# Performance work log

Hardware: AMD Instinct MI355X
Metric: run time of the kernel (lower is better)

The kernel has to match this reference:

```python
import jax, jax.numpy as jnp
import numpy as np

SP = 1024; H = 128; W = 128; BAND = 224; DIM = 256; HEADS = 8; DH = 64; HID = 512; NS = 6
SCALE = DH ** -0.5

def setup_inputs() -> dict:
    key = jax.random.key(0)
    ks = iter(jax.random.split(key, 48))
    def rn(shape, s=0.02):
        return jax.random.normal(next(ks), shape, dtype=jnp.float32) * s
    # pixel -> superpixel one-hot assignment; every column nonempty so C_T division is safe
    Q = jax.nn.one_hot(jnp.arange(H * W) % SP, SP, dtype=jnp.float32)
    A = rn((SP, SP), 0.1)  # additive attention bias (graph prior)
    T1 = jax.random.normal(next(ks), (1, BAND, H, W), dtype=jnp.float32)
    T2 = jax.random.normal(next(ks), (1, BAND, H, W), dtype=jnp.float32)
    return {
        "T1": T1, "T2": T2, "Q": Q, "A": A,
        "convW_in": rn((2, 256, BAND, 3, 3)), "convB_in": jnp.zeros((2, 256), jnp.float32),
        "convW": rn((5, 2, 256, 256, 3, 3)), "convB": jnp.zeros((5, 2, 256), jnp.float32),
        "fc0_W": rn((2, BAND + 256, 256)), "fc0_b": jnp.zeros((2, 256), jnp.float32),
        "fc_W": rn((5, 2, 512, 256)), "fc_b": jnp.zeros((5, 2, 256), jnp.float32),
        "pos": rn((NS, 2, SP, DIM)),
        "ln1_g": jnp.ones((NS, 2, DIM), jnp.float32), "ln1_b": jnp.zeros((NS, 2, DIM), jnp.float32),
        "qkv_W": rn((NS, 2, DIM, 3 * HEADS * DH)),
        "out_W": rn((NS, 2, HEADS * DH, DIM)), "out_b": jnp.zeros((NS, 2, DIM), jnp.float32),
        "ln2_g": jnp.ones((NS, 2, DIM), jnp.float32), "ln2_b": jnp.zeros((NS, 2, DIM), jnp.float32),
        "ff_W1": rn((NS, 2, DIM, HID)), "ff_b1": jnp.zeros((NS, 2, HID), jnp.float32),
        "ff_W2": rn((NS, 2, HID, DIM)), "ff_b2": jnp.zeros((NS, 2, DIM), jnp.float32),
        "head_W1": rn((DIM, 128)), "head_b1": jnp.zeros((128,), jnp.float32),
        "head_W2": rn((128, 2)), "head_b2": jnp.zeros((2,), jnp.float32),
    }

def _ln(x, g, b):
    m = jnp.mean(x, -1, keepdims=True)
    v = jnp.mean((x - m) ** 2, -1, keepdims=True)
    return (x - m) * jax.lax.rsqrt(v + 1e-5) * g + b

def _conv(x, w, b):
    y = jax.lax.conv_general_dilated(x, w, (1, 1), 'SAME', dimension_numbers=('NCHW', 'OIHW', 'NCHW'))
    return y + b[None, :, None, None]

def _ct(Q, img):
    # superpixel mean pooling: (Q^T @ pixels) / |superpixel|
    band = img.shape[1]
    x = jnp.transpose(img, (0, 2, 3, 1)).reshape(-1, band)  # (HW, band)
    out = (Q.T @ x) / jnp.sum(Q, axis=0)[:, None]
    return out[None]  # (1, SP, band)

def _encoder(x, A, pos, g1, b1, qkvW, oW, ob, g2, b2, w1, bb1, w2, bb2):
    x = x + pos[None]
    h = _ln(x, g1, b1)
    q, k, v = jnp.split(h @ qkvW, 3, axis=-1)
    split = lambda t: t.reshape(1, SP, HEADS, DH).transpose(0, 2, 1, 3)
    q, k, v = split(q), split(k), split(v)
    dots = jnp.einsum('bhid,bhjd->bhij', q, k) * SCALE + A  # bias added pre-softmax
    attn = jax.nn.softmax(dots, axis=-1)
    o = jnp.einsum('bhij,bhjd->bhid', attn, v).transpose(0, 2, 1, 3).reshape(1, SP, HEADS * DH)
    x = x + o @ oW + ob
    h2 = _ln(x, g2, b2)
    return x + jax.nn.gelu(h2 @ w1 + bb1, approximate=False) @ w2 + bb2

def reference(T1, T2, Q, A, convW_in, convB_in, convW, convB, fc0_W, fc0_b, fc_W, fc_b, pos, ln1_g, ln1_b, qkv_W, out_W, out_b, ln2_g, ln2_b, ff_W1, ff_b1, ff_W2, ff_b2, head_W1, head_b1, head_W2, head_b2):
    def enc(t, s, br):
        return _encoder(t, A, pos[s, br], ln1_g[s, br], ln1_b[s, br], qkv_W[s, br], out_W[s, br], out_b[s, br], ln2_g[s, br], ln2_b[s, br], ff_W1[s, br], ff_b1[s, br], ff_W2[s, br], ff_b2[s, br])
    LS = [_ct(Q, T1), _ct(Q, T2)]
    c = [_conv(T1, convW_in[0], convB_in[0]), _conv(T2, convW_in[1], convB_in[1])]
    x = [None, None]
    for br in range(2):
        cat = jnp.concatenate([_ct(Q, c[br]), LS[br]], axis=-1)  # (1, SP, 256+224)
        x[br] = enc(jax.nn.relu(cat) @ fc0_W[br] + fc0_b[br], 0, br)
    for s in range(1, NS):
        for br in range(2):
            c[br] = _conv(c[br], convW[s - 1, br], convB[s - 1, br])
            cat = jnp.concatenate([_ct(Q, c[br]), x[br]], axis=-1)  # (1, SP, 512)
            x[br] = enc(jax.nn.relu(cat) @ fc_W[s - 1, br] + fc_b[s - 1, br], s, br)
    d = jnp.abs(x[0] - x[1])[0]  # (SP, DIM) change feature
    h = jax.nn.relu(d @ head_W1 + head_b1)
    return jax.nn.softmax(h @ head_W2 + head_b2, axis=1)  # (SP, 2)
```

## Files before the change

### kernel.cpp

```cpp
#include <hip/hip_runtime.h>
#include <hip/hip_bf16.h>
#include <math.h>

#define SPX 1024
#define HW 16384

typedef short short8 __attribute__((ext_vector_type(8)));
typedef short short4v __attribute__((ext_vector_type(4)));
typedef float f32x4 __attribute__((ext_vector_type(4)));

__device__ inline short f2bf(float v){ union{ __hip_bfloat16 h; short s; } u; u.h = __float2bfloat16(v); return u.s; }
__device__ inline float bf2f(short s){ union{ __hip_bfloat16 h; short t; } u; u.t = s; return __bfloat162float(u.h); }

#define GLL(gp, lp) __builtin_amdgcn_global_load_lds( \
    (const __attribute__((address_space(1))) void*)(gp), \
    (__attribute__((address_space(3))) void*)(lp), 16, 0, 0)

__global__ __launch_bounds__(256) void megaprep_k(
    const float* __restrict__ T1, const float* __restrict__ T2,
    const float* __restrict__ cwin, const float* __restrict__ cw,
    const float* __restrict__ qkvW, const float* __restrict__ outW,
    const float* __restrict__ ff1W, const float* __restrict__ ff2W,
    const float* __restrict__ fcW, const float* __restrict__ fc0W,
    short* __restrict__ wt0, short* __restrict__ wtl, short* __restrict__ zbuf,
    short* __restrict__ thwc, float* __restrict__ LSb,
    short* __restrict__ qkvWT, short* __restrict__ outWT,
    short* __restrict__ ff1T, short* __restrict__ ff2T,
    short* __restrict__ fcT, short* __restrict__ fc0WT)
{
    __shared__ float tile[32][33];
    int bid = blockIdx.x;
    int tid = threadIdx.x;
    if (bid < 27072) {
        long long idx = (long long)bid * 256 + tid;
        if (idx < 64) zbuf[idx] = 0;
        const long long n0 = 2LL * 256 * 2016;
        if (idx < n0) {
            int br = (int)(idx / (256 * 2016)); int rem = (int)(idx % (256 * 2016));
            int co = rem / 2016; int k = rem % 2016;
            int tap = k / 224, ci = k % 224;
            wt0[idx] = f2bf(cwin[((size_t)(br * 256 + co) * 224 + ci) * 9 + tap]);
        } else {
            long long i2 = idx - n0;
            if (i2 < 10LL * 256 * 2304) {
                int l = (int)(i2 / (256 * 2304)); int rem = (int)(i2 % (256 * 2304));
                int co = rem / 2304; int k = rem % 2304;
                int tap = k / 256, ci = k % 256;
                wtl[i2] = f2bf(cw[((size_t)(l * 256 + co) * 256 + ci) * 9 + tap]);
            }
        }
        return;
    }
    bid -= 27072;
    if (bid < 28672) {
        long long idx = (long long)bid * 256 + tid;
        int br = (int)(idx / 3670016LL); int rem = (int)(idx % 3670016LL);
        int p = rem / 224, c = rem % 224;
        const float* src = br ? T2 : T1;
        thwc[idx] = f2bf(src[(size_t)c * HW + p]);
        return;
    }
    bid -= 28672;
    if (bid < 1792) {
        int idx = bid * 256 + tid;
        int z = idx / 229376; int rem = idx % 229376;
        int c = rem >> 10, s = rem & 1023;
        const float* src = z ? T2 : T1;
        const float* p = src + (size_t)c * HW + s;
        float acc = 0.f;
#pragma unroll
        for (int j = 0; j < 16; ++j) acc += p[j * 1024];
        LSb[(size_t)z * 229376 + (size_t)s * 224 + c] = acc * (1.f / 16.f);
        return;
    }
    bid -= 1792;
    const float* src; short* dst; int K, N, nx;
    if (bid < 4608)                        { src = qkvW; dst = qkvWT; K = 256; N = 1536; nx = 48; }
    else { bid -= 4608; if (bid < 1536)    { src = outW; dst = outWT; K = 512; N = 256;  nx = 8; }
    else { bid -= 1536; if (bid < 1536)    { src = ff1W; dst = ff1T;  K = 256; N = 512;  nx = 16; }
    else { bid -= 1536; if (bid < 1536)    { src = ff2W; dst = ff2T;  K = 512; N = 256;  nx = 8; }
    else { bid -= 1536; if (bid < 1280)    { src = fcW;  dst = fcT;   K = 512; N = 256;  nx = 8; }
    else { bid -= 1280;                      src = fc0W; dst = fc0WT; K = 480; N = 256;  nx = 8; } } } } }
    int per = nx * (K >> 5);
    int b = bid / per, rem = bid % per;
    int n0 = (rem % nx) * 32, k0 = (rem / nx) * 32;
    const float* s = src + (size_t)b * K * N;
    short* d = dst + (size_t)b * K * N;
    int r = tid >> 3, c4 = (tid & 7) * 4;
    float4 v = *(const float4*)(s + (size_t)(k0 + r) * N + n0 + c4);
    tile[r][c4 + 0] = v.x; tile[r][c4 + 1] = v.y; tile[r][c4 + 2] = v.z; tile[r][c4 + 3] = v.w;
    __syncthreads();
    short4v o;
#pragma unroll
    for (int i = 0; i < 4; ++i) o[i] = f2bf(tile[c4 + i][r]);
    *(short4v*)(d + (size_t)(n0 + r) * K + k0 + c4) = o;
}

__global__ __launch_bounds__(256, 3) void conv_mfma_k(
    const short* __restrict__ inB, long long inStride,
    const short* __restrict__ wtB, long long wtStride,
    const float* __restrict__ biasB, long long biasStride,
    short* __restrict__ outB, long long outStride,
    const short* __restrict__ zbuf, int Cin)
{
    __shared__ short Ah[3 * 4160];
    int id = blockIdx.x;
    int x7 = id & 7, t = id >> 3;
    int br = x7 & 1;
    int y = (x7 >> 1) * 32 + (t >> 1);
    int co0 = (t & 1) * 128;
    const short* in = inB + (size_t)br * inStride;
    const short* wt = wtB + (size_t)br * wtStride;
    const float* bias = biasB + (size_t)br * biasStride;
    short* out = outB + (size_t)br * outStride;
    int tid = threadIdx.x;
    int lane = tid & 63, w = tid >> 6;
    int wm = w >> 1, wn = w & 1;
    int lrow = lane >> 2, lsub = (lane & 3) * 8;
    int mrow = lane & 15, quad = lane >> 4, kg = quad * 8;
    int Kw = 9 * Cin;
    if (tid < 96) {
        int dy = tid >> 5, ci = tid & 31;
        Ah[dy * 4160 + ci] = 0;
        Ah[dy * 4160 + 129 * 32 + ci] = 0;
    }
    f32x4 acc[4][4];
#pragma unroll
    for (int i = 0; i < 4; ++i)
#pragma unroll
        for (int j = 0; j < 4; ++j) acc[i][j] = (f32x4){0.f, 0.f, 0.f, 0.f};

    const short* wbase[4];
#pragma unroll
    for (int j = 0; j < 4; ++j)
        wbase[j] = wt + (size_t)(co0 + wn * 64 + j * 16 + mrow) * Kw + kg;

    auto stageA = [&](int cc) {
        int c8 = cc * 32;
#pragma unroll
        for (int g = 0; g < 6; ++g) {
            int idg = g * 4 + w;
            int dy = idg >> 3, grp = idg & 7;
            int gy = y + dy - 1;
            const short* gp = ((unsigned)gy < 128u)
                ? in + ((size_t)(gy * 128 + grp * 16 + lrow) * Cin + c8 + lsub)
                : zbuf + lsub;
            GLL(gp, Ah + dy * 4160 + (1 + grp * 16) * 32);
        }
    };

    short8 Bcur[4], Bnxt[4];
#pragma unroll
    for (int j = 0; j < 4; ++j) Bcur[j] = *(const short8*)(wbase[j]);
    stageA(0);
    __syncthreads();
    int NC = Cin >> 5;
    for (int cc = 0; cc < NC; ++cc) {
        int cbase = cc * 32;
#pragma unroll
        for (int tap = 0; tap < 9; ++tap) {
            if (tap < 8) {
#pragma unroll
                for (int j = 0; j < 4; ++j)
                    Bnxt[j] = *(const short8*)(wbase[j] + (tap + 1) * Cin + cbase);
            } else if (cc + 1 < NC) {
#pragma unroll
                for (int j = 0; j < 4; ++j)
                    Bnxt[j] = *(const short8*)(wbase[j] + cbase + 32);
            }
            const short* Ap = Ah + (tap / 3) * 4160 + (tap % 3) * 32;
            short8 af[4];
#pragma unroll
            for (int i = 0; i < 4; ++i)
                af[i] = *(const short8*)(Ap + (wm * 64 + i * 16 + mrow) * 32 + kg);
#pragma unroll
            for (int i = 0; i < 4; ++i)
#pragma unroll
                for (int j = 0; j < 4; ++j)
                    acc[i][j] = __builtin_amdgcn_mfma_f32_16x16x32_bf16(af[i], Bcur[j], acc[i][j], 0, 0, 0);
#pragma unroll
            for (int j = 0; j < 4; ++j) Bcur[j] = Bnxt[j];
        }
        if (cc + 1 < NC) {
            __syncthreads();
            stageA(cc + 1);
            __syncthreads();
        }
    }
    int ln15 = lane & 15;
    float bj[4];
#pragma unroll
    for (int j = 0; j < 4; ++j) bj[j] = bias[co0 + wn * 64 + j * 16 + ln15];
#pragma unroll
    for (int i = 0; i < 4; ++i) {
#pragma unroll
        for (int r = 0; r < 4; ++r) {
            int px = wm * 64 + i * 16 + quad * 4 + r;
            size_t po = ((size_t)y * 128 + px) * 256 + co0 + wn * 64 + ln15;
#pragma unroll
            for (int j = 0; j < 4; ++j)
                out[po + j * 16] = f2bf(acc[i][j][r] + bj[j]);
        }
    }
}

__global__ __launch_bounds__(256) void gemm64_k(
    const short* __restrict__ A, long long sA, int lda,
    const short* __restrict__ Bt, long long sB, int K,
    float* Cf, long long sCf, short* Cb, long long sCb, int ldc,
    const float* __restrict__ bias, long long sBias,
    const float* addm, long long sAdd, int ldadd, int act)
{
    __shared__ short Asm[2][2048];
    __shared__ short Bsm[2][2048];
    int z = blockIdx.z;
    const short* Ap = A + (size_t)z * sA;
    const short* Bp = Bt + (size_t)z * sB;
    const float* biasp = bias ? bias + (size_t)z * sBias : nullptr;
    const float* addp = addm ? addm + (size_t)z * sAdd : nullptr;
    int bn = blockIdx.x * 64, bm = blockIdx.y * 64;
    int tid = threadIdx.x;
    int lane = tid & 63, w = tid >> 6;
    int wm = w >> 1, wn = w & 1;
    int rr = tid >> 2, lsub = (tid & 3) * 8;
    f32x4 acc[2][2];
#pragma unroll
    for (int i = 0; i < 2; ++i)
#pragma unroll
        for (int j = 0; j < 2; ++j) acc[i][j] = (f32x4){0.f, 0.f, 0.f, 0.f};

    auto stage = [&](int k0, int p) {
        GLL(Ap + (size_t)(bm + rr) * lda + k0 + lsub, Asm[p] + (w * 16) * 32);
        GLL(Bp + (size_t)(bn + rr) * K + k0 + lsub, Bsm[p] + (w * 16) * 32);
    };
    stage(0, 0);
    __syncthreads();
    int p = 0;
    int mrow = lane & 15, kg = (lane >> 4) * 8;
    for (int k0 = 0; k0 < K; k0 += 32) {
        if (k0 + 32 < K) stage(k0 + 32, p ^ 1);
        short8 af[2], bfr[2];
#pragma unroll
        for (int i = 0; i < 2; ++i)
            af[i] = *(const short8*)(Asm[p] + (wm * 32 + i * 16 + mrow) * 32 + kg);
#pragma unroll
        for (int j = 0; j < 2; ++j)
            bfr[j] = *(const short8*)(Bsm[p] + (wn * 32 + j * 16 + mrow) * 32 + kg);
#pragma unroll
        for (int i = 0; i < 2; ++i)
#pragma unroll
            for (int j = 0; j < 2; ++j)
                acc[i][j] = __builtin_amdgcn_mfma_f32_16x16x32_bf16(af[i], bfr[j], acc[i][j], 0, 0, 0);
        __syncthreads();
        p ^= 1;
    }
    int ln15 = lane & 15, quad = lane >> 4;
    float* Cfp = Cf ? Cf + (size_t)z * sCf : nullptr;
    short* Cbp = Cb ? Cb + (size_t)z * sCb : nullptr;
#pragma unroll
    for (int i = 0; i < 2; ++i) {
#pragma unroll
        for (int r = 0; r < 4; ++r) {
            int row = bm + wm * 32 + i * 16 + quad * 4 + r;
            long long ro = (long long)row * ldc;
#pragma unroll
            for (int j = 0; j < 2; ++j) {
                int col = bn + wn * 32 + j * 16 + ln15;
                float v = acc[i][j][r];
                if (biasp) v += biasp[col];
                if (addp) v += addp[(long long)row * ldadd + col];
                if (act == 1) v = fmaxf(v, 0.f);
                else if (act == 2) v = 0.5f * v * (1.f + erff(v * 0.70710678118f));
                if (Cfp) Cfp[ro + col] = v;
                if (Cbp) Cbp[ro + col] = f2bf(v);
            }
        }
    }
}

__global__ __launch_bounds__(256) void gemm_ln_k(
    const short* __restrict__ A, long long sA, int lda,
    const short* __restrict__ Bt, long long sB, int K,
    const float* __restrict__ bias, long long sBias,
    const float* __restrict__ addm, long long sAdd,
    const float* __restrict__ g, const float* __restrict__ b,
    float* __restrict__ xout, long long sX, short* __restrict__ hout, long long sH)
{
    __shared__ short As[2][512];
    __shared__ short Bsm[2][8192];
    __shared__ float redS[16][4], redQ[16][4];
    int z = blockIdx.y;
    int bm = blockIdx.x * 16;
    const short* Ap = A + (size_t)z * sA;
    const short* Bp = Bt + (size_t)z * sB;
    const float* biasp = bias + (size_t)z * sBias;
    const float* addp = addm + (size_t)z * sAdd;
    const float* gp = g + (size_t)z * 256;
    const float* bp = b + (size_t)z * 256;
    float* xo = xout + (size_t)z * sX;
    short* ho = hout + (size_t)z * sH;
    int tid = threadIdx.x;
    int lane = tid & 63, w = tid >> 6;
    int lrow = lane >> 2, lsub = (lane & 3) * 8;
    int mrow = lane & 15, quad = lane >> 4, kg = quad * 8;
    f32x4 acc[4];
#pragma unroll
    for (int j = 0; j < 4; ++j) acc[j] = (f32x4){0.f, 0.f, 0.f, 0.f};

    auto stage = [&](int k0, int p) {
        if (w == 0) GLL(Ap + (size_t)(bm + lrow) * lda + k0 + lsub, As[p]);
#pragma unroll
        for (int s = 0; s < 4; ++s) {
            int r0 = (w * 4 + s) * 16;
            GLL(Bp + (size_t)(r0 + lrow) * K + k0 + lsub, Bsm[p] + r0 * 32);
        }
    };
    stage(0, 0);
    __syncthreads();
    int NK = K >> 5, p = 0;
    for (int kk = 0; kk < NK; ++kk) {
        if (kk + 1 < NK) stage((kk + 1) * 32, p ^ 1);
        short8 af = *(const short8*)(As[p] + mrow * 32 + kg);
#pragma unroll
        for (int j = 0; j < 4; ++j) {
            short8 bfr = *(const short8*)(Bsm[p] + (w * 64 + j * 16 + mrow) * 32 + kg);
            acc[j] = __builtin_amdgcn_mfma_f32_16x16x32_bf16(af, bfr, acc[j], 0, 0, 0);
        }
        __syncthreads();
        p ^= 1;
    }
    float v[4][4], s4[4], q4[4];
#pragma unroll
    for (int r = 0; r < 4; ++r) { s4[r] = 0.f; q4[r] = 0.f; }
#pragma unroll
    for (int j = 0; j < 4; ++j) {
        int col = w * 64 + j * 16 + mrow;
        float bb = biasp[col];
#pragma unroll
        for (int r = 0; r < 4; ++r) {
            int row = bm + quad * 4 + r;
            float val = acc[j][r] + bb + addp[(size_t)row * 256 + col];
            v[j][r] = val;
            s4[r] += val;
            q4[r] += val * val;
        }
    }
#pragma unroll
    for (int r = 0; r < 4; ++r) {
#pragma unroll
        for (int msk = 1; msk < 16; msk <<= 1) {
            s4[r] += __shfl_xor(s4[r], msk);
            q4[r] += __shfl_xor(q4[r], msk);
        }
    }
    if (mrow == 0) {
#pragma unroll
        for (int r = 0; r < 4; ++r) {
            redS[quad * 4 + r][w] = s4[r];
            redQ[quad * 4 + r][w] = q4[r];
        }
    }
    __syncthreads();
#pragma unroll
    for (int r = 0; r < 4; ++r) {
        int r16 = quad * 4 + r;
        float S = redS[r16][0] + redS[r16][1] + redS[r16][2] + redS[r16][3];
        float Q = redQ[r16][0] + redQ[r16][1] + redQ[r16][2] + redQ[r16][3];
        float m = S * (1.f / 256.f);
        float var = Q * (1.f / 256.f) - m * m;
        float rs = rsqrtf(var + 1e-5f);
        size_t ro = (size_t)(bm + r16) * 256;
#pragma unroll
        for (int j = 0; j < 4; ++j) {
            int col = w * 64 + j * 16 + mrow;
            xo[ro + col] = v[j][r];
            ho[ro + col] = f2bf((v[j][r] - m) * rs * gp[col] + bp[col]);
        }
    }
}

__global__ __launch_bounds__(256) void flash_k(const short* __restrict__ qkv, const float* __restrict__ Abias,
                                               short* __restrict__ obuf)
{
    __shared__ short Qs[64 * 72];
    __shared__ short Ks[128 * 72];
    __shared__ short Vt[64 * 136];
    __shared__ short Ps[64 * 136];
    int q0 = blockIdx.x * 64, h = blockIdx.y, br = blockIdx.z;
    const short* qb = qkv + (size_t)br * 1572864;
    int tid = threadIdx.x;
    int lane = tid & 63, w = tid >> 6;
    int ln15 = lane & 15, quad = lane >> 4;
    {
        int row = tid & 63, c0 = (tid >> 6) * 16;
        const short* src = qb + (size_t)(q0 + row) * 1536 + h * 64 + c0;
        *(short8*)(Qs + row * 72 + c0) = *(const short8*)src;
        *(short8*)(Qs + row * 72 + c0 + 8) = *(const short8*)(src + 8);
    }
    f32x4 Oc[4];
    float mrow[4], lsum[4];
#pragma unroll
    for (int i = 0; i < 4; ++i) { Oc[i] = (f32x4){0.f, 0.f, 0.f, 0.f}; mrow[i] = -1e30f; lsum[i] = 0.f; }

    for (int j = 0; j < 8; ++j) {
        int k0 = j * 128;
        {
            int row = tid & 127, half = tid >> 7;
            const short* ks = qb + (size_t)(k0 + row) * 1536 + 512 + h * 64 + half * 32;
#pragma unroll
            for (int g = 0; g < 4; ++g)
                *(short8*)(Ks + row * 72 + half * 32 + g * 8) = *(const short8*)(ks + g * 8);
            const short* vs = qb + (size_t)(k0 + row) * 1536 + 1024 + h * 64 + half * 32;
#pragma unroll
            for (int g = 0; g < 4; ++g) {
                short8 vv = *(const short8*)(vs + g * 8);
#pragma unroll
                for (int e = 0; e < 8; ++e)
                    Vt[(half * 32 + g * 8 + e) * 136 + row] = vv[e];
            }
        }
        __syncthreads();
        short8 aq[2];
#pragma unroll
        for (int g = 0; g < 2; ++g)
            aq[g] = *(const short8*)(Qs + (w * 16 + ln15) * 72 + g * 32 + quad * 8);
        f32x4 Sf[8];
#pragma unroll
        for (int nf = 0; nf < 8; ++nf) Sf[nf] = (f32x4){0.f, 0.f, 0.f, 0.f};
#pragma unroll
        for (int nf = 0; nf < 8; ++nf)
#pragma unroll
            for (int g = 0; g < 2; ++g) {
                short8 bk = *(const short8*)(Ks + (nf * 16 + ln15) * 72 + g * 32 + quad * 8);
                Sf[nf] = __builtin_amdgcn_mfma_f32_16x16x32_bf16(aq[g], bk, Sf[nf], 0, 0, 0);
            }
        float rm[4] = {-1e30f, -1e30f, -1e30f, -1e30f};
#pragma unroll
        for (int nf = 0; nf < 8; ++nf)
#pragma unroll
            for (int r = 0; r < 4; ++r) {
                float v = Sf[nf][r] * 0.125f +
                          Abias[(size_t)(q0 + w * 16 + quad * 4 + r) * 1024 + k0 + nf * 16 + ln15];
                Sf[nf][r] = v;
                rm[r] = fmaxf(rm[r], v);
            }
#pragma unroll
        for (int r = 0; r < 4; ++r)
#pragma unroll
            for (int msk = 1; msk < 16; msk <<= 1)
                rm[r] = fmaxf(rm[r], __shfl_xor(rm[r], msk));
        float alpha[4], rs[4];
#pragma unroll
        for (int r = 0; r < 4; ++r) {
            float mnew = fmaxf(mrow[r], rm[r]);
            alpha[r] = __expf(mrow[r] - mnew);
            mrow[r] = mnew;
            rs[r] = 0.f;
        }
#pragma unroll
        for (int nf = 0; nf < 8; ++nf)
#pragma unroll
            for (int r = 0; r < 4; ++r) {
                float pv = __expf(Sf[nf][r] - mrow[r]);
                Sf[nf][r] = pv;
                rs[r] += pv;
            }
#pragma unroll
        for (int r = 0; r < 4; ++r) {
#pragma unroll
            for (int msk = 1; msk < 16; msk <<= 1)
                rs[r] += __shfl_xor(rs[r], msk);
            lsum[r] = lsum[r] * alpha[r] + rs[r];
        }
#pragma unroll
        for (int nf = 0; nf < 4; ++nf)
#pragma unroll
            for (int r = 0; r < 4; ++r) Oc[nf][r] *= alpha[r];
#pragma unroll
        for (int nf = 0; nf < 8; ++nf)
#pragma unroll
            for (int r = 0; r < 4; ++r)
                Ps[(w * 16 + quad * 4 + r) * 136 + nf * 16 + ln15] = f2bf(Sf[nf][r]);
        __syncthreads();
#pragma unroll
        for (int g = 0; g < 4; ++g) {
            short8 ap = *(const short8*)(Ps + (w * 16 + ln15) * 136 + g * 32 + quad * 8);
#pragma unroll
            for (int nf = 0; nf < 4; ++nf) {
                short8 bv = *(const short8*)(Vt + (nf * 16 + ln15) * 136 + g * 32 + quad * 8);
                Oc[nf] = __builtin_amdgcn_mfma_f32_16x16x32_bf16(ap, bv, Oc[nf], 0, 0, 0);
            }
        }
        __syncthreads();
    }
#pragma unroll
    for (int nf = 0; nf < 4; ++nf)
#pragma unroll
        for (int r = 0; r < 4; ++r) {
            int row = q0 + w * 16 + quad * 4 + r;
            obuf[(size_t)br * 524288 + (size_t)row * 512 + h * 64 + nf * 16 + ln15] =
                f2bf(Oc[nf][r] / lsum[r]);
        }
}

__global__ __launch_bounds__(256) void poolcat_k(const short* __restrict__ conv, long long convZ,
                                                 const float* __restrict__ bsrc, long long bZ, int cb,
                                                 short* __restrict__ catr, long long catZ)
{
    int row = blockIdx.x, z = blockIdx.y, tid = threadIdx.x;
    const short* p = conv + (size_t)z * convZ + (size_t)row * 256 + tid;
    float acc = 0.f;
#pragma unroll
    for (int j = 0; j < 16; ++j) acc += bf2f(p[(size_t)j * 262144]);
    int n = 256 + cb;
    short* op = catr + (size_t)z * catZ + (size_t)row * n;
    op[tid] = f2bf(fmaxf(acc * (1.f / 16.f), 0.f));
    if (tid < cb)
        op[256 + tid] = f2bf(fmaxf(bsrc[(size_t)z * bZ + (size_t)row * cb + tid], 0.f));
}

__global__ __launch_bounds__(256) void head1_k(const float* __restrict__ x0, const float* __restrict__ x1,
                                               const float* __restrict__ B, float* __restrict__ C,
                                               const float* __restrict__ bias)
{
    __shared__ __align__(16) float As[16][68];
    __shared__ __align__(16) float Bs[16][68];
    const int K = 256, lda = 256, ldb = 128, ldc = 128;
    int bn = blockIdx.x * 64, bm = blockIdx.y * 64;
    int tid = threadIdx.x;
    int tx = tid & 15, ty = tid >> 4;
    float acc[4][4];
#pragma unroll
    for (int r = 0; r < 4; ++r)
#pragma unroll
        for (int c = 0; c < 4; ++c) acc[r][c] = 0.f;
    int mmA = tid >> 2, kqA = (tid & 3) * 4;
    int kkB = tid >> 4, nqB = (tid & 15) * 4;
    for (int k0 = 0; k0 < K; k0 += 16) {
        float4 a0 = *(const float4*)(x0 + (long long)(bm + mmA) * lda + k0 + kqA);
        float4 a1 = *(const float4*)(x1 + (long long)(bm + mmA) * lda + k0 + kqA);
        As[kqA + 0][mmA] = fabsf(a0.x - a1.x); As[kqA + 1][mmA] = fabsf(a0.y - a1.y);
        As[kqA + 2][mmA] = fabsf(a0.z - a1.z); As[kqA + 3][mmA] = fabsf(a0.w - a1.w);
        *(float4*)&Bs[kkB][nqB] = *(const float4*)(B + (long long)(k0 + kkB) * ldb + bn + nqB);
        __syncthreads();
#pragma unroll
        for (int kk = 0; kk < 16; ++kk) {
            float4 a4 = *(const float4*)&As[kk][ty * 4];
            float4 b4 = *(const float4*)&Bs[kk][tx * 4];
            float ar[4] = {a4.x, a4.y, a4.z, a4.w};
            float br[4] = {b4.x, b4.y, b4.z, b4.w};
#pragma unroll
            for (int r = 0; r < 4; ++r)
#pragma unroll
                for (int c = 0; c < 4; ++c) acc[r][c] += ar[r] * br[c];
        }
        __syncthreads();
    }
#pragma unroll
    for (int r = 0; r < 4; ++r) {
        int row = bm + ty * 4 + r;
#pragma unroll
        for (int c = 0; c < 4; ++c) {
            int col = bn + tx * 4 + c;
            C[(long long)row * ldc + col] = fmaxf(acc[r][c] + bias[col], 0.f);
        }
    }
}

__global__ __launch_bounds__(256) void head2_k(const float* __restrict__ hh, const float* __restrict__ W2,
                                               const float* __restrict__ b2, float* __restrict__ out)
{
    int s = blockIdx.x * 256 + threadIdx.x;
    if (s >= SPX) return;
    float l0 = b2[0], l1 = b2[1];
    const float* hp = hh + (size_t)s * 128;
    for (int k = 0; k < 128; ++k) {
        float v = hp[k];
        l0 += v * W2[k * 2];
        l1 += v * W2[k * 2 + 1];
    }
    float m = fmaxf(l0, l1);
    float e0 = __expf(l0 - m), e1 = __expf(l1 - m);
    float inv = 1.f / (e0 + e1);
    out[s * 2] = e0 * inv;
    out[s * 2 + 1] = e1 * inv;
}

extern "C" void kernel_launch(void* const* d_in, const int* in_sizes, int n_in,
                              void* d_out, int out_size, void* d_ws, size_t ws_size,
                              hipStream_t stream)
{
    (void)in_sizes; (void)n_in; (void)out_size; (void)ws_size;
    const float* T1 = (const float*)d_in[0];
    const float* T2 = (const float*)d_in[1];
    const float* Abias = (const float*)d_in[3];
    const float* convW_in = (const float*)d_in[4];
    const float* convB_in = (const float*)d_in[5];
    const float* convW = (const float*)d_in[6];
    const float* convB = (const float*)d_in[7];
    const float* fc0_W = (const float*)d_in[8];
    const float* fc0_b = (const float*)d_in[9];
    const float* fc_W = (const float*)d_in[10];
    const float* fc_b = (const float*)d_in[11];
    const float* pos = (const float*)d_in[12];
    const float* ln1_g = (const float*)d_in[13];
    const float* ln1_b = (const float*)d_in[14];
    const float* qkv_W = (const float*)d_in[15];
    const float* out_W = (const float*)d_in[16];
    const float* out_b = (const float*)d_in[17];
    const float* ln2_g = (const float*)d_in[18];
    const float* ln2_b = (const float*)d_in[19];
    const float* ff_W1 = (const float*)d_in[20];
    const float* ff_b1 = (const float*)d_in[21];
    const float* ff_W2 = (const float*)d_in[22];
    const float* ff_b2 = (const float*)d_in[23];
    const float* head_W1 = (const float*)d_in[24];
    const float* head_b1 = (const float*)d_in[25];
    const float* head_W2 = (const float*)d_in[26];
    const float* head_b2 = (const float*)d_in[27];
    float* outp = (float*)d_out;

    char* wp = (char*)d_ws;
    auto alloc = [&](size_t bytes) { char* p = wp; wp += (bytes + 255) & ~(size_t)255; return p; };
    short* cbufA = (short*)alloc(16777216);
    short* cbufB = (short*)alloc(16777216);
    short* wt0   = (short*)alloc(2064384);
    short* wtl   = (short*)alloc(11796480);
    short* zbuf  = (short*)alloc(256);
    short* thwc  = (short*)alloc(14680064);
    short* qkvWT = (short*)alloc(9437184);
    short* outWT = (short*)alloc(3145728);
    short* ff1T  = (short*)alloc(3145728);
    short* ff2T  = (short*)alloc(3145728);
    short* fcT   = (short*)alloc(2621440);
    short* fc0WT = (short*)alloc(245760);
    short* qkvb  = (short*)alloc(6291456);
    short* obuf  = (short*)alloc(2097152);
    short* hbuf  = (short*)alloc(1048576);
    short* h2b   = (short*)alloc(1048576);
    short* ffhb  = (short*)alloc(2097152);
    short* catr  = (short*)alloc(2097152);
    float* LSb    = (float*)alloc(1835008);
    float* xbuf   = (float*)alloc(2097152);
    float* hhb    = (float*)alloc(524288);

    auto gemm = [&](const short* A, long long sA, int lda, const short* Bt, long long sB,
                    int N, int K, float* Cf, long long sCf, short* Cb, long long sCb, int ldc,
                    const float* bias, long long sBias, const float* addm, long long sAdd, int ldadd, int act) {
        gemm64_k<<<dim3((unsigned)(N / 64), 16, 2), 256, 0, stream>>>(
            A, sA, lda, Bt, sB, K, Cf, sCf, Cb, sCb, ldc, bias, sBias, addm, sAdd, ldadd, act);
    };

    megaprep_k<<<68272, 256, 0, stream>>>(T1, T2, convW_in, convW, qkv_W, out_W, ff_W1, ff_W2,
                                          fc_W, fc0_W, wt0, wtl, zbuf, thwc, LSb,
                                          qkvWT, outWT, ff1T, ff2T, fcT, fc0WT);

    conv_mfma_k<<<512, 256, 0, stream>>>(thwc, 3670016LL, wt0, 516096LL, convB_in, 256LL,
                                         cbufA, 4194304LL, zbuf, 224);
    short* cur = cbufA; short* nxt = cbufB;
    for (int s = 0; s < 6; ++s) {
        if (s > 0) {
            conv_mfma_k<<<512, 256, 0, stream>>>(cur, 4194304LL, wtl + (size_t)(s - 1) * 2 * 589824,
                                                 589824LL, convB + (size_t)(s - 1) * 512, 256LL,
                                                 nxt, 4194304LL, zbuf, 256);
            short* t = cur; cur = nxt; nxt = t;
        }
        if (s == 0) {
            poolcat_k<<<dim3(1024, 2), 256, 0, stream>>>(cur, 4194304LL, LSb, 229376LL, 224, catr, 491520LL);
            gemm_ln_k<<<dim3(64, 2), 256, 0, stream>>>(
                catr, 491520LL, 480, fc0WT, 122880LL, 480, fc0_b, 256LL,
                pos, 262144LL, ln1_g, ln1_b, xbuf, 262144LL, hbuf, 262144LL);
        } else {
            poolcat_k<<<dim3(1024, 2), 256, 0, stream>>>(cur, 4194304LL, xbuf, 262144LL, 256, catr, 524288LL);
            gemm_ln_k<<<dim3(64, 2), 256, 0, stream>>>(
                catr, 524288LL, 512, fcT + (size_t)(s - 1) * 262144, 131072LL, 512,
                fc_b + (size_t)(s - 1) * 512, 256LL,
                pos + (size_t)s * 524288, 262144LL, ln1_g + s * 512, ln1_b + s * 512,
                xbuf, 262144LL, hbuf, 262144LL);
        }
        gemm(hbuf, 262144, 256, qkvWT + (size_t)s * 786432, 393216, 1536, 256,
             nullptr, 0, qkvb, 1572864, 1536, nullptr, 0, nullptr, 0, 0, 0);
        flash_k<<<dim3(16, 8, 2), 256, 0, stream>>>(qkvb, Abias, obuf);
        gemm_ln_k<<<dim3(64, 2), 256, 0, stream>>>(
            obuf, 524288LL, 512, outWT + (size_t)s * 262144, 131072LL, 512,
            out_b + s * 512, 256LL, xbuf, 262144LL, ln2_g + s * 512, ln2_b + s * 512,
            xbuf, 262144LL, h2b, 262144LL);
        gemm(h2b, 262144, 256, ff1T + (size_t)s * 262144, 131072, 512, 256,
             nullptr, 0, ffhb, 524288, 512, ff_b1 + s * 1024, 512, nullptr, 0, 0, 2);
        gemm(ffhb, 524288, 512, ff2T + (size_t)s * 262144, 131072, 256, 512, xbuf, 262144,
             nullptr, 0, 256, ff_b2 + s * 512, 256, xbuf, 262144, 256, 0);
    }
    head1_k<<<dim3(2, 16), 256, 0, stream>>>(xbuf, xbuf + 262144, head_W1, hhb, head_b1);
    head2_k<<<4, 256, 0, stream>>>(hhb, head_W2, head_b2, outp);
}
```

Measured before the change: 1.310 ms.

## Stage conv weights through double-buffered LDS and tile-transpose input prep

The conv kernel no longer loads weight fragments straight from global memory into registers. Each tap's 128x32 weight slice is now staged into a double-buffered shared-memory tile with global_load_lds and read back as MFMA fragments, with a barrier after every tap. The occupancy hint of 3 blocks per SM is dropped from the launch bounds. Separately, the NCHW-to-HWC bf16 conversion in the prep kernel now uses a 32x32 shared-memory tile transpose with float4 reads and vectorised writes instead of scattered per-element strided loads, which reduces its grid size. The per-tap barriers and extra shared memory may reduce overlap and occupancy.

```diff
diff --git a/kernel.cpp b/kernel.cpp
--- a/kernel.cpp
+++ b/kernel.cpp
@@ -52,15 +52,21 @@
         return;
     }
     bid -= 27072;
-    if (bid < 28672) {
-        long long idx = (long long)bid * 256 + tid;
-        int br = (int)(idx / 3670016LL); int rem = (int)(idx % 3670016LL);
-        int p = rem / 224, c = rem % 224;
+    if (bid < 7168) {
+        int br = bid / 3584, rem2 = bid % 3584;
+        int p0 = (rem2 / 7) * 32, c0 = (rem2 % 7) * 32;
         const float* src = br ? T2 : T1;
-        thwc[idx] = f2bf(src[(size_t)c * HW + p]);
+        int r = tid >> 3, c4 = (tid & 7) * 4;
+        float4 v = *(const float4*)(src + (size_t)(c0 + r) * HW + p0 + c4);
+        tile[r][c4 + 0] = v.x; tile[r][c4 + 1] = v.y; tile[r][c4 + 2] = v.z; tile[r][c4 + 3] = v.w;
+        __syncthreads();
+        short4v o;
+#pragma unroll
+        for (int i = 0; i < 4; ++i) o[i] = f2bf(tile[c4 + i][r]);
+        *(short4v*)(thwc + (size_t)br * 3670016 + (size_t)(p0 + r) * 224 + c0 + c4) = o;
         return;
     }
-    bid -= 28672;
+    bid -= 7168;
     if (bid < 1792) {
         int idx = bid * 256 + tid;
         int z = idx / 229376; int rem = idx % 229376;
@@ -96,7 +102,7 @@
     *(short4v*)(d + (size_t)(n0 + r) * K + k0 + c4) = o;
 }
 
-__global__ __launch_bounds__(256, 3) void conv_mfma_k(
+__global__ __launch_bounds__(256) void conv_mfma_k(
     const short* __restrict__ inB, long long inStride,
     const short* __restrict__ wtB, long long wtStride,
     const float* __restrict__ biasB, long long biasStride,
@@ -104,6 +110,7 @@
     const short* __restrict__ zbuf, int Cin)
 {
     __shared__ short Ah[3 * 4160];
+    __shared__ short Bs[2][4096];
     int id = blockIdx.x;
     int x7 = id & 7, t = id >> 3;
     int br = x7 & 1;
@@ -117,7 +124,6 @@
     int lane = tid & 63, w = tid >> 6;
     int wm = w >> 1, wn = w & 1;
     int lrow = lane >> 2, lsub = (lane & 3) * 8;
-    int mrow = lane & 15, quad = lane >> 4, kg = quad * 8;
     int Kw = 9 * Cin;
     if (tid < 96) {
         int dy = tid >> 5, ci = tid & 31;
@@ -129,11 +135,6 @@
     for (int i = 0; i < 4; ++i)
 #pragma unroll
         for (int j = 0; j < 4; ++j) acc[i][j] = (f32x4){0.f, 0.f, 0.f, 0.f};
-
-    const short* wbase[4];
-#pragma unroll
-    for (int j = 0; j < 4; ++j)
-        wbase[j] = wt + (size_t)(co0 + wn * 64 + j * 16 + mrow) * Kw + kg;
 
     auto stageA = [&](int cc) {
         int c8 = cc * 32;
@@ -148,46 +149,50 @@
             GLL(gp, Ah + dy * 4160 + (1 + grp * 16) * 32);
         }
     };
-
-    short8 Bcur[4], Bnxt[4];
-#pragma unroll
-    for (int j = 0; j < 4; ++j) Bcur[j] = *(const short8*)(wbase[j]);
+    auto stageB = [&](int cc, int tap, int p) {
+        int c8 = cc * 32;
+#pragma unroll
+        for (int s = 0; s < 2; ++s) {
+            int r0 = (s * 4 + w) * 16;
+            const short* gq = wt + ((size_t)(co0 + r0 + lrow) * Kw + tap * Cin + c8 + lsub);
+            GLL(gq, Bs[p] + r0 * 32);
+        }
+    };
+
     stageA(0);
+    stageB(0, 0, 0);
     __syncthreads();
     int NC = Cin >> 5;
+    int pb = 0;
+    int mrow = lane & 15, kg = (lane >> 4) * 8;
     for (int cc = 0; cc < NC; ++cc) {
-        int cbase = cc * 32;
 #pragma unroll
         for (int tap = 0; tap < 9; ++tap) {
-            if (tap < 8) {
-#pragma unroll
-                for (int j = 0; j < 4; ++j)
-                    Bnxt[j] = *(const short8*)(wbase[j] + (tap + 1) * Cin + cbase);
-            } else if (cc + 1 < NC) {
-#pragma unroll
-                for (int j = 0; j < 4; ++j)
-                    Bnxt[j] = *(const short8*)(wbase[j] + cbase + 32);
-            }
-            const short* Ap = Ah + (tap / 3) * 4160 + (tap % 3) * 32;
-            short8 af[4];
+            if (tap < 8) stageB(cc, tap + 1, pb ^ 1);
+            else if (cc + 1 < NC) stageB(cc + 1, 0, pb ^ 1);
+            int ky = tap / 3, kx = tap % 3;
+            const short* Ap = Ah + ky * 4160 + kx * 32;
+            short8 af[4], bfr[4];
 #pragma unroll
             for (int i = 0; i < 4; ++i)
                 af[i] = *(const short8*)(Ap + (wm * 64 + i * 16 + mrow) * 32 + kg);
 #pragma unroll
+            for (int j = 0; j < 4; ++j)
+                bfr[j] = *(const short8*)(Bs[pb] + (wn * 64 + j * 16 + mrow) * 32 + kg);
+#pragma unroll
             for (int i = 0; i < 4; ++i)
 #pragma unroll
                 for (int j = 0; j < 4; ++j)
-                    acc[i][j] = __builtin_amdgcn_mfma_f32_16x16x32_bf16(af[i], Bcur[j], acc[i][j], 0, 0, 0);
-#pragma unroll
-            for (int j = 0; j < 4; ++j) Bcur[j] = Bnxt[j];
+                    acc[i][j] = __builtin_amdgcn_mfma_f32_16x16x32_bf16(af[i], bfr[j], acc[i][j], 0, 0, 0);
+            __syncthreads();
+            pb ^= 1;
         }
         if (cc + 1 < NC) {
-            __syncthreads();
             stageA(cc + 1);
             __syncthreads();
         }
     }
-    int ln15 = lane & 15;
+    int ln15 = lane & 15, quad = lane >> 4;
     float bj[4];
 #pragma unroll
     for (int j = 0; j < 4; ++j) bj[j] = bias[co0 + wn * 64 + j * 16 + ln15];
@@ -651,7 +656,7 @@
             A, sA, lda, Bt, sB, K, Cf, sCf, Cb, sCb, ldc, bias, sBias, addm, sAdd, ldadd, act);
     };
 
-    megaprep_k<<<68272, 256, 0, stream>>>(T1, T2, convW_in, convW, qkv_W, out_W, ff_W1, ff_W2,
+    megaprep_k<<<46768, 256, 0, stream>>>(T1, T2, convW_in, convW, qkv_W, out_W, ff_W1, ff_W2,
                                           fc_W, fc0_W, wt0, wtl, zbuf, thwc, LSb,
                                           qkvWT, outWT, ff1T, ff2T, fcT, fc0WT);
 
```

New measurement: 1.117 ms. -14.7%, faster.
